# Kernel tuning notes

Measured on AMD Instinct MI355X. Metric: run time of the kernel, lower is better.

The kernel has to match this reference:

```python
import jax, jax.numpy as jnp
import numpy as np

N, E, F_IN, H, L = 1536, 49152, 27, 64, 32


def _ln(x, g, b, eps=1e-5):
    m = x.mean(-1, keepdims=True)
    v = ((x - m) ** 2).mean(-1, keepdims=True)
    return (x - m) * jax.lax.rsqrt(v + eps) * g + b


def _gatv2(x, src, dst, Wl, bl, Wr, br, att, bias, n):
    # PyG GATv2Conv, heads=1: alpha_ij = softmax_j( att . leaky_relu(Wl x_j + Wr x_i) )
    xl = x @ Wl + bl  # source transform [n,H]
    xr = x @ Wr + br  # target transform [n,H]
    e = jax.nn.leaky_relu(xl[src] + xr[dst], 0.2)  # [E',H]
    s = e @ att  # [E'] attention logits
    m = jax.ops.segment_max(s, dst, num_segments=n)
    w = jnp.exp(s - m[dst])
    denom = jax.ops.segment_sum(w, dst, num_segments=n)
    alpha = w / denom[dst]
    return jax.ops.segment_sum(alpha[:, None] * xl[src], dst, num_segments=n) + bias


def _model(x, eps_nodes, eps_graph, edge_index,
           Wl1, bl1, Wr1, br1, att1, bias1,
           Wl2, bl2, Wr2, br2, att2, bias2,
           Wnm, bnm, Wnv, bnv, Wgm, bgm, Wgv, bgv,
           Wd1, bd1, ln1_g, ln1_b, Wd2, bd2, ln2_g, ln2_b, Wd3, bd3,
           We1, be1, lne_g, lne_b, We2, be2,
           Wf1, bf1, lnf_g, lnf_b, Wf2, bf2):
    n = x.shape[0]
    loop = jnp.arange(n)
    src = jnp.concatenate([edge_index[0], loop])  # add self loops (PyG default)
    dst = jnp.concatenate([edge_index[1], loop])
    h = jax.nn.relu(_gatv2(x, src, dst, Wl1, bl1, Wr1, br1, att1, bias1, n))
    h = jax.nn.relu(_gatv2(h, src, dst, Wl2, bl2, Wr2, br2, att2, bias2, n))
    node_mu = h @ Wnm + bnm
    node_logvar = h @ Wnv + bnv
    gh = h.mean(0)
    graph_mu = gh @ Wgm + bgm
    graph_logvar = gh @ Wgv + bgv
    z = node_mu + eps_nodes * jnp.exp(0.5 * node_logvar)  # node reparam (training)
    _zg = graph_mu + eps_graph * jnp.exp(0.5 * graph_logvar)  # z_graph: computed, unused downstream as in source
    # dec_node_features MLP
    nf = _ln(jax.nn.relu(z @ Wd1 + bd1), ln1_g, ln1_b)
    nf = _ln(jax.nn.relu(nf @ Wd2 + bd2), ln2_g, ln2_b)
    nf = nf @ Wd3 + bd3  # [n, F_IN]
    # feature_refinement (node_embeddings = h is passed in forward)
    nf = _ln(jax.nn.relu(jnp.concatenate([nf, h], -1) @ Wf1 + bf1), lnf_g, lnf_b)
    node_features = nf @ Wf2 + bf2
    # edge_pred over all i<j pairs, vectorized (replaces the O(N^2) python loop)
    iu, ju = jnp.triu_indices(n, k=1)
    ei = jnp.concatenate([z[iu], z[ju]], -1)  # [P, 2L]
    eh = _ln(jax.nn.relu(ei @ We1 + be1), lne_g, lne_b)
    edge_logits = (eh @ We2 + be2)[:, 0]  # [P]
    return node_features, edge_logits, node_mu, node_logvar, graph_mu, graph_logvar


def setup_inputs() -> dict:
    key = jax.random.key(0)
    ki = iter(jax.random.split(key, 40))
    def W(fi, fo):
        return jax.random.normal(next(ki), (fi, fo), jnp.float32) / np.sqrt(fi)
    z64 = jnp.zeros((H,), jnp.float32)
    o64 = jnp.ones((H,), jnp.float32)
    zL = jnp.zeros((L,), jnp.float32)
    zF = jnp.zeros((F_IN,), jnp.float32)
    inp = {}
    inp["x"] = jax.random.normal(next(ki), (N, F_IN), jnp.float32)
    inp["edge_index"] = jax.random.randint(next(ki), (2, E), 0, N)
    inp["eps_nodes"] = jax.random.normal(next(ki), (N, L), jnp.float32)
    inp["eps_graph"] = jax.random.normal(next(ki), (L,), jnp.float32)
    inp.update(Wl1=W(F_IN, H), bl1=z64, Wr1=W(F_IN, H), br1=z64,
               att1=jax.random.normal(next(ki), (H,), jnp.float32) / np.sqrt(H), bias1=z64,
               Wl2=W(H, H), bl2=z64, Wr2=W(H, H), br2=z64,
               att2=jax.random.normal(next(ki), (H,), jnp.float32) / np.sqrt(H), bias2=z64)
    inp.update(Wnm=W(H, L), bnm=zL, Wnv=W(H, L), bnv=zL,
               Wgm=W(H, L), bgm=zL, Wgv=W(H, L), bgv=zL)
    inp.update(Wd1=W(L, H), bd1=z64, ln1_g=o64, ln1_b=z64,
               Wd2=W(H, H), bd2=z64, ln2_g=o64, ln2_b=z64,
               Wd3=W(H, F_IN), bd3=zF)
    inp.update(We1=W(2 * L, H), be1=z64, lne_g=o64, lne_b=z64,
               We2=W(H, 1), be2=jnp.zeros((1,), jnp.float32))
    inp.update(Wf1=W(F_IN + H, H), bf1=z64, lnf_g=o64, lnf_b=z64,
               Wf2=W(H, F_IN), bf2=zF)
    return inp


def reference(x, edge_index, eps_nodes, eps_graph,
              Wl1, bl1, Wr1, br1, att1, bias1,
              Wl2, bl2, Wr2, br2, att2, bias2,
              Wnm, bnm, Wnv, bnv, Wgm, bgm, Wgv, bgv,
              Wd1, bd1, ln1_g, ln1_b, Wd2, bd2, ln2_g, ln2_b, Wd3, bd3,
              We1, be1, lne_g, lne_b, We2, be2,
              Wf1, bf1, lnf_g, lnf_b, Wf2, bf2):
    return _model(x, eps_nodes, eps_graph, edge_index,
                  Wl1, bl1, Wr1, br1, att1, bias1,
                  Wl2, bl2, Wr2, br2, att2, bias2,
                  Wnm, bnm, Wnv, bnv, Wgm, bgm, Wgv, bgv,
                  Wd1, bd1, ln1_g, ln1_b, Wd2, bd2, ln2_g, ln2_b, Wd3, bd3,
                  We1, be1, lne_g, lne_b, We2, be2,
                  Wf1, bf1, lnf_g, lnf_b, Wf2, bf2)
```

## Files before the change

kernel.cpp:

```cpp
#include <hip/hip_runtime.h>

#define NN 1536
#define NE 49152
#define FIN 27
#define HD 64
#define LDIM 32
#define PP 1178880
#define CAP 128

#define EL_OFF  (NN*FIN)
#define MU_OFF  (EL_OFF + PP)
#define LV_OFF  (MU_OFF + NN*LDIM)
#define GMU_OFF (LV_OFF + NN*LDIM)
#define GLV_OFF (GMU_OFF + LDIM)

__device__ __forceinline__ float wsum(float v) {
#pragma unroll
  for (int m = 1; m < 64; m <<= 1) v += __shfl_xor(v, m, 64);
  return v;
}
__device__ __forceinline__ void wsum2(float& a, float& b) {
#pragma unroll
  for (int m = 1; m < 64; m <<= 1) {
    a += __shfl_xor(a, m, 64);
    b += __shfl_xor(b, m, 64);
  }
}
__device__ __forceinline__ void wsum4(float& a, float& b, float& c, float& d) {
#pragma unroll
  for (int m = 1; m < 64; m <<= 1) {
    a += __shfl_xor(a, m, 64);
    b += __shfl_xor(b, m, 64);
    c += __shfl_xor(c, m, 64);
    d += __shfl_xor(d, m, 64);
  }
}
__device__ __forceinline__ float lnorm64(float x, float g, float b) {
  float s1 = x, s2 = x * x;
  wsum2(s1, s2);
  float mu = s1 * (1.0f / 64.0f);
  float var = fmaf(-mu, mu, s2 * (1.0f / 64.0f));
  return (x - mu) * rsqrtf(var + 1e-5f) * g + b;
}
__device__ __forceinline__ void cp4(float* dst, const float* __restrict__ src,
                                    int n4, int t) {
  const float4* s4 = (const float4*)src;
  float4* d4 = (float4*)dst;
  for (int e = t; e < n4; e += 256) d4[e] = s4[e];
}

__device__ __forceinline__ float gat_gather(const int* __restrict__ cnt,
                                            const int* __restrict__ slot,
                                            const float* __restrict__ xl,
                                            float xri, float ak, int i, int k) {
  int n = min(cnt[i], CAP);
  const int* srow = slot + i * CAP;
  float acc = 0.f, den = 0.f;
  for (int e0 = 0; e0 < n; e0 += 64) {
    int sidx = (e0 + k < n) ? srow[e0 + k] : 0;
    int nn = min(64, n - e0);
    int j = 0;
    for (; j + 3 < nn; j += 4) {
      int s0 = __shfl(sidx, j, 64),     s1 = __shfl(sidx, j + 1, 64);
      int s2 = __shfl(sidx, j + 2, 64), s3 = __shfl(sidx, j + 3, 64);
      float x0 = xl[s0 * HD + k], x1 = xl[s1 * HD + k];
      float x2 = xl[s2 * HD + k], x3 = xl[s3 * HD + k];
      float e0v = x0 + xri, e1v = x1 + xri, e2v = x2 + xri, e3v = x3 + xri;
      e0v = fmaxf(e0v, 0.2f * e0v);
      e1v = fmaxf(e1v, 0.2f * e1v);
      e2v = fmaxf(e2v, 0.2f * e2v);
      e3v = fmaxf(e3v, 0.2f * e3v);
      float p0 = e0v * ak, p1 = e1v * ak, p2 = e2v * ak, p3 = e3v * ak;
      wsum4(p0, p1, p2, p3);
      float w0 = expf(p0), w1 = expf(p1), w2 = expf(p2), w3 = expf(p3);
      acc = fmaf(w0, x0, acc); den += w0;
      acc = fmaf(w1, x1, acc); den += w1;
      acc = fmaf(w2, x2, acc); den += w2;
      acc = fmaf(w3, x3, acc); den += w3;
    }
    for (; j < nn; ++j) {
      int s0 = __shfl(sidx, j, 64);
      float x0 = xl[s0 * HD + k];
      float e0v = x0 + xri;
      e0v = fmaxf(e0v, 0.2f * e0v);
      float w0 = expf(wsum(e0v * ak));
      acc = fmaf(w0, x0, acc); den += w0;
    }
  }
  float xs = xl[i * HD + k];
  float es = xs + xri;
  es = fmaxf(es, 0.2f * es);
  float ws = expf(wsum(es * ak));
  acc = fmaf(ws, xs, acc); den += ws;
  return acc / den;
}

__global__ __launch_bounds__(256) void gvae_xform1(
    const float* __restrict__ in,
    const float* __restrict__ Wl, const float* __restrict__ bl,
    const float* __restrict__ Wr, const float* __restrict__ br,
    float* __restrict__ xl, float* __restrict__ xr,
    const int* __restrict__ ei, int* __restrict__ cnt, int* __restrict__ slot) {
  __shared__ __align__(16) float sWl[FIN * HD];
  __shared__ __align__(16) float sWr[FIN * HD];
  int t = threadIdx.x;
  int gid = blockIdx.x * 256 + t;
  if (gid < NE) {
    int d = ei[NE + gid];
    int c = atomicAdd(&cnt[d], 1);
    if (c < CAP) slot[d * CAP + c] = ei[gid];
  }
  cp4(sWl, Wl, FIN * 16, t);
  cp4(sWr, Wr, FIN * 16, t);
  int i = blockIdx.x * 4 + (t >> 6);
  int k = t & 63;
  float xv = (k < FIN) ? in[i * FIN + k] : 0.f;
  float l0 = bl[k], l1 = 0.f, r0 = br[k], r1 = 0.f;
  __syncthreads();
#pragma unroll
  for (int a = 0; a < FIN; a += 2) {
    float xa = __shfl(xv, a, 64);
    l0 = fmaf(xa, sWl[a * HD + k], l0);
    r0 = fmaf(xa, sWr[a * HD + k], r0);
    if (a + 1 < FIN) {
      float xb = __shfl(xv, a + 1, 64);
      l1 = fmaf(xb, sWl[(a + 1) * HD + k], l1);
      r1 = fmaf(xb, sWr[(a + 1) * HD + k], r1);
    }
  }
  xl[i * HD + k] = l0 + l1;
  xr[i * HD + k] = r0 + r1;
}

__global__ __launch_bounds__(256) void gvae_gatherx(
    const int* __restrict__ cnt, const int* __restrict__ slot,
    const float* __restrict__ xl, const float* __restrict__ xr,
    const float* __restrict__ att, const float* __restrict__ hbias,
    const float* __restrict__ Wl, const float* __restrict__ bl,
    const float* __restrict__ Wr, const float* __restrict__ br,
    float* __restrict__ xlo, float* __restrict__ xro) {
  int t = threadIdx.x;
  int i = blockIdx.x * 4 + (t >> 6);
  int k = t & 63;
  float xri = xr[i * HD + k];
  float ak = att[k];
  float hv = fmaxf(gat_gather(cnt, slot, xl, xri, ak, i, k) + hbias[k], 0.f);
  float l0 = bl[k], l1 = 0.f, r0 = br[k], r1 = 0.f;
#pragma unroll
  for (int a = 0; a < HD; a += 2) {
    float xa = __shfl(hv, a, 64);
    float xb = __shfl(hv, a + 1, 64);
    l0 = fmaf(xa, Wl[a * HD + k], l0);
    r0 = fmaf(xa, Wr[a * HD + k], r0);
    l1 = fmaf(xb, Wl[(a + 1) * HD + k], l1);
    r1 = fmaf(xb, Wr[(a + 1) * HD + k], r1);
  }
  xlo[i * HD + k] = l0 + l1;
  xro[i * HD + k] = r0 + r1;
}

__global__ __launch_bounds__(256, 4) void gvae_node(
    const int* __restrict__ cnt, const int* __restrict__ slot,
    const float* __restrict__ xl, const float* __restrict__ xr,
    const float* __restrict__ att, const float* __restrict__ bias2,
    const float* __restrict__ eps,
    const float* __restrict__ Wnm, const float* __restrict__ bnm,
    const float* __restrict__ Wnv, const float* __restrict__ bnv,
    const float* __restrict__ We1, const float* __restrict__ be1,
    const float* __restrict__ Wd1, const float* __restrict__ bd1,
    const float* __restrict__ g1, const float* __restrict__ b1,
    const float* __restrict__ Wd2, const float* __restrict__ bd2,
    const float* __restrict__ g2, const float* __restrict__ b2,
    const float* __restrict__ Wd3, const float* __restrict__ bd3,
    const float* __restrict__ Wf1, const float* __restrict__ bf1,
    const float* __restrict__ gf, const float* __restrict__ bfv,
    const float* __restrict__ Wf2, const float* __restrict__ bf2,
    float* __restrict__ uo, float* __restrict__ vo,
    float* __restrict__ gh, float* __restrict__ out) {
  __shared__ float ghred[256];
  int t = threadIdx.x;
  int i = blockIdx.x * 4 + (t >> 6);
  int k = t & 63;
  int kk = k & 31;
  int kc = (k < FIN) ? k : (FIN - 1);

  float xri = xr[i * HD + k];
  float ak = att[k];
  float h2k = fmaxf(gat_gather(cnt, slot, xl, xri, ak, i, k) + bias2[k], 0.f);
  ghred[t] = h2k;
  __syncthreads();
  if (t < 64) {
    float s = (ghred[t] + ghred[t + 64]) + (ghred[t + 128] + ghred[t + 192]);
    atomicAdd(&gh[t], s * (1.0f / NN));
  }

  const float* W = (k < 32) ? Wnm : Wnv;
  float c0 = (k < 32) ? bnm[kk] : bnv[kk];
  float c1 = 0.f, c2 = 0.f, c3 = 0.f;
#pragma unroll
  for (int a = 0; a < HD; a += 4) {
    c0 = fmaf(__shfl(h2k, a, 64),     W[a * LDIM + kk],       c0);
    c1 = fmaf(__shfl(h2k, a + 1, 64), W[(a + 1) * LDIM + kk], c1);
    c2 = fmaf(__shfl(h2k, a + 2, 64), W[(a + 2) * LDIM + kk], c2);
    c3 = fmaf(__shfl(h2k, a + 3, 64), W[(a + 3) * LDIM + kk], c3);
  }
  float acc = (c0 + c1) + (c2 + c3);
  if (k < 32) out[MU_OFF + i * LDIM + kk] = acc;
  else        out[LV_OFF + i * LDIM + kk] = acc;

  float lv = __shfl(acc, k + 32, 64);
  float zk = acc + eps[i * LDIM + kk] * expf(0.5f * lv);

  float u0 = be1[k], u1 = 0.f, v0 = 0.f, v1 = 0.f;
#pragma unroll
  for (int a = 0; a < LDIM; a += 2) {
    float za = __shfl(zk, a, 64);
    float zb = __shfl(zk, a + 1, 64);
    u0 = fmaf(za, We1[a * HD + k], u0);
    u1 = fmaf(zb, We1[(a + 1) * HD + k], u1);
    v0 = fmaf(za, We1[(a + LDIM) * HD + k], v0);
    v1 = fmaf(zb, We1[(a + 1 + LDIM) * HD + k], v1);
  }
  uo[i * HD + k] = u0 + u1;
  vo[i * HD + k] = v0 + v1;

  c0 = bd1[k]; c1 = 0.f; c2 = 0.f; c3 = 0.f;
#pragma unroll
  for (int a = 0; a < LDIM; a += 4) {
    c0 = fmaf(__shfl(zk, a, 64),     Wd1[a * HD + k],       c0);
    c1 = fmaf(__shfl(zk, a + 1, 64), Wd1[(a + 1) * HD + k], c1);
    c2 = fmaf(__shfl(zk, a + 2, 64), Wd1[(a + 2) * HD + k], c2);
    c3 = fmaf(__shfl(zk, a + 3, 64), Wd1[(a + 3) * HD + k], c3);
  }
  float nf1 = lnorm64(fmaxf((c0 + c1) + (c2 + c3), 0.f), g1[k], b1[k]);

  c0 = bd2[k]; c1 = 0.f; c2 = 0.f; c3 = 0.f;
#pragma unroll
  for (int a = 0; a < HD; a += 4) {
    c0 = fmaf(__shfl(nf1, a, 64),     Wd2[a * HD + k],       c0);
    c1 = fmaf(__shfl(nf1, a + 1, 64), Wd2[(a + 1) * HD + k], c1);
    c2 = fmaf(__shfl(nf1, a + 2, 64), Wd2[(a + 2) * HD + k], c2);
    c3 = fmaf(__shfl(nf1, a + 3, 64), Wd2[(a + 3) * HD + k], c3);
  }
  float nf2 = lnorm64(fmaxf((c0 + c1) + (c2 + c3), 0.f), g2[k], b2[k]);

  c0 = 0.f; c1 = 0.f; c2 = 0.f; c3 = 0.f;
#pragma unroll
  for (int a = 0; a < HD; a += 4) {
    c0 = fmaf(__shfl(nf2, a, 64),     Wd3[a * FIN + kc],       c0);
    c1 = fmaf(__shfl(nf2, a + 1, 64), Wd3[(a + 1) * FIN + kc], c1);
    c2 = fmaf(__shfl(nf2, a + 2, 64), Wd3[(a + 2) * FIN + kc], c2);
    c3 = fmaf(__shfl(nf2, a + 3, 64), Wd3[(a + 3) * FIN + kc], c3);
  }
  float nf3 = (k < FIN) ? ((c0 + c1) + (c2 + c3) + bd3[kc]) : 0.f;

  c0 = bf1[k]; c1 = 0.f; c2 = 0.f; c3 = 0.f;
#pragma unroll
  for (int j = 0; j < FIN; j++) {
    float nj = __shfl(nf3, j, 64);
    c0 = fmaf(nj, Wf1[j * HD + k], c0);
  }
#pragma unroll
  for (int a = 0; a < HD; a += 4) {
    c0 = fmaf(__shfl(h2k, a, 64),     Wf1[(FIN + a) * HD + k],     c0);
    c1 = fmaf(__shfl(h2k, a + 1, 64), Wf1[(FIN + a + 1) * HD + k], c1);
    c2 = fmaf(__shfl(h2k, a + 2, 64), Wf1[(FIN + a + 2) * HD + k], c2);
    c3 = fmaf(__shfl(h2k, a + 3, 64), Wf1[(FIN + a + 3) * HD + k], c3);
  }
  float rr = lnorm64(fmaxf((c0 + c1) + (c2 + c3), 0.f), gf[k], bfv[k]);

  c0 = 0.f; c1 = 0.f; c2 = 0.f; c3 = 0.f;
#pragma unroll
  for (int a = 0; a < HD; a += 4) {
    c0 = fmaf(__shfl(rr, a, 64),     Wf2[a * FIN + kc],       c0);
    c1 = fmaf(__shfl(rr, a + 1, 64), Wf2[(a + 1) * FIN + kc], c1);
    c2 = fmaf(__shfl(rr, a + 2, 64), Wf2[(a + 2) * FIN + kc], c2);
    c3 = fmaf(__shfl(rr, a + 3, 64), Wf2[(a + 3) * FIN + kc], c3);
  }
  if (k < FIN) out[i * FIN + k] = (c0 + c1) + (c2 + c3) + bf2[kc];
}

__global__ __launch_bounds__(256) void gvae_edge(
    const float* __restrict__ u, const float* __restrict__ v,
    const float* __restrict__ lng, const float* __restrict__ lnb,
    const float* __restrict__ w2, const float* __restrict__ be2,
    const float* __restrict__ gh,
    const float* __restrict__ Wgm, const float* __restrict__ bgm,
    const float* __restrict__ Wgv, const float* __restrict__ bgv,
    float* __restrict__ out) {
  __shared__ float U[64 * 64];
  __shared__ float V[64 * 68];
  __shared__ float C[64];
  __shared__ float cc[2];
  int t = threadIdx.x;
  int wv = t >> 6, lane = t & 63;

  if (blockIdx.x == 0 && wv == 3) {
    int kk = lane & 31;
    float ghk = gh[lane];
    const float* W = (lane < 32) ? Wgm : Wgv;
    float c0 = (lane < 32) ? bgm[kk] : bgv[kk];
    float c1 = 0.f, c2 = 0.f, c3 = 0.f;
#pragma unroll
    for (int a = 0; a < HD; a += 4) {
      c0 = fmaf(__shfl(ghk, a, 64),     W[a * LDIM + kk],       c0);
      c1 = fmaf(__shfl(ghk, a + 1, 64), W[(a + 1) * LDIM + kk], c1);
      c2 = fmaf(__shfl(ghk, a + 2, 64), W[(a + 2) * LDIM + kk], c2);
      c3 = fmaf(__shfl(ghk, a + 3, 64), W[(a + 3) * LDIM + kk], c3);
    }
    float acc = (c0 + c1) + (c2 + c3);
    if (lane < 32) out[GMU_OFF + kk] = acc;
    else           out[GLV_OFF + kk] = acc;
  }

  int rem = blockIdx.x, bi = 0;
  while (rem >= 24 - bi) { rem -= 24 - bi; bi++; }
  int bj = bi + rem;

  const float4* u4p = (const float4*)(u + bi * 64 * HD);
  const float4* v4p = (const float4*)(v + bj * 64 * HD);
#pragma unroll
  for (int it = 0; it < 4; ++it) {
    int r = t + it * 256;
    int row = r >> 4, q = r & 15;
    float4 uu = u4p[r];
    *(float4*)&U[row * 64 + q * 4] = uu;
    float4 vv = v4p[r];
    *(float4*)&V[row * 68 + q * 4] = vv;
  }
  if (t < 64) {
    float ck = lng[t] * w2[t];
    C[t] = ck;
    float cb = lnb[t] * w2[t];
    float sC = wsum(ck);
    float sB = wsum(cb);
    if (t == 0) { cc[0] = sC; cc[1] = sB + be2[0]; }
  }
  __syncthreads();
  float C1 = cc[0], C0 = cc[1];

  float S1[16], S2[16], Sc[16];
#pragma unroll
  for (int ii = 0; ii < 16; ii++) { S1[ii] = 0.f; S2[ii] = 0.f; Sc[ii] = 0.f; }
  const float* Ub = &U[(wv * 16) * 64];
  for (int k4 = 0; k4 < 16; k4++) {
    float4 v4 = *(const float4*)&V[lane * 68 + k4 * 4];
    float4 c4 = *(const float4*)&C[k4 * 4];
#pragma unroll
    for (int ii = 0; ii < 16; ii++) {
      float4 u4 = *(const float4*)&Ub[ii * 64 + k4 * 4];
      float t0 = fmaxf(u4.x + v4.x, 0.f);
      float t1 = fmaxf(u4.y + v4.y, 0.f);
      float t2 = fmaxf(u4.z + v4.z, 0.f);
      float t3 = fmaxf(u4.w + v4.w, 0.f);
      S1[ii] += (t0 + t1) + (t2 + t3);
      S2[ii] = fmaf(t0, t0, fmaf(t1, t1, fmaf(t2, t2, fmaf(t3, t3, S2[ii]))));
      Sc[ii] = fmaf(t0, c4.x, fmaf(t1, c4.y, fmaf(t2, c4.z, fmaf(t3, c4.w, Sc[ii]))));
    }
  }
  int j = bj * 64 + lane;
  const float inv64 = 1.0f / 64.0f;
#pragma unroll
  for (int ii = 0; ii < 16; ii++) {
    int i = bi * 64 + wv * 16 + ii;
    if (j > i) {
      int pbase = i * (2 * NN - i - 1) / 2 - i - 1;
      float mu = S1[ii] * inv64;
      float var = fmaf(-mu, mu, S2[ii] * inv64);
      float logit = (Sc[ii] - mu * C1) * rsqrtf(var + 1e-5f) + C0;
      out[EL_OFF + pbase + j] = logit;
    }
  }
}

extern "C" void kernel_launch(void* const* d_in, const int* in_sizes, int n_in,
                              void* d_out, int out_size, void* d_ws, size_t ws_size,
                              hipStream_t stream) {
  const float* x    = (const float*)d_in[0];
  const int*   ei   = (const int*)d_in[1];
  const float* eps  = (const float*)d_in[2];
  const float* Wl1  = (const float*)d_in[4];
  const float* bl1  = (const float*)d_in[5];
  const float* Wr1  = (const float*)d_in[6];
  const float* br1  = (const float*)d_in[7];
  const float* att1 = (const float*)d_in[8];
  const float* bias1= (const float*)d_in[9];
  const float* Wl2  = (const float*)d_in[10];
  const float* bl2  = (const float*)d_in[11];
  const float* Wr2  = (const float*)d_in[12];
  const float* br2  = (const float*)d_in[13];
  const float* att2 = (const float*)d_in[14];
  const float* bias2= (const float*)d_in[15];
  const float* Wnm  = (const float*)d_in[16];
  const float* bnm  = (const float*)d_in[17];
  const float* Wnv  = (const float*)d_in[18];
  const float* bnv  = (const float*)d_in[19];
  const float* Wgm  = (const float*)d_in[20];
  const float* bgm  = (const float*)d_in[21];
  const float* Wgv  = (const float*)d_in[22];
  const float* bgv  = (const float*)d_in[23];
  const float* Wd1  = (const float*)d_in[24];
  const float* bd1  = (const float*)d_in[25];
  const float* ln1g = (const float*)d_in[26];
  const float* ln1b = (const float*)d_in[27];
  const float* Wd2  = (const float*)d_in[28];
  const float* bd2  = (const float*)d_in[29];
  const float* ln2g = (const float*)d_in[30];
  const float* ln2b = (const float*)d_in[31];
  const float* Wd3  = (const float*)d_in[32];
  const float* bd3  = (const float*)d_in[33];
  const float* We1  = (const float*)d_in[34];
  const float* be1  = (const float*)d_in[35];
  const float* lneg = (const float*)d_in[36];
  const float* lneb = (const float*)d_in[37];
  const float* We2  = (const float*)d_in[38];
  const float* be2  = (const float*)d_in[39];
  const float* Wf1  = (const float*)d_in[40];
  const float* bf1  = (const float*)d_in[41];
  const float* lnfg = (const float*)d_in[42];
  const float* lnfb = (const float*)d_in[43];
  const float* Wf2  = (const float*)d_in[44];
  const float* bf2  = (const float*)d_in[45];
  float* out = (float*)d_out;

  float* fb  = (float*)d_ws;
  float* xl1 = fb;
  float* xr1 = xl1 + NN * HD;
  float* xl2 = xr1 + NN * HD;
  float* xr2 = xl2 + NN * HD;
  float* uu  = xr2 + NN * HD;
  float* vv  = uu  + NN * HD;
  float* gh  = vv  + NN * HD;
  int* cnt    = (int*)(gh + HD);
  int* slot   = cnt + NN;

  hipMemsetAsync(gh, 0, (HD + NN) * sizeof(float), stream);

  gvae_xform1<<<NN / 4, 256, 0, stream>>>(x, Wl1, bl1, Wr1, br1, xl1, xr1,
                                          ei, cnt, slot);
  gvae_gatherx<<<NN / 4, 256, 0, stream>>>(cnt, slot, xl1, xr1, att1, bias1,
                                           Wl2, bl2, Wr2, br2, xl2, xr2);
  gvae_node<<<NN / 4, 256, 0, stream>>>(cnt, slot, xl2, xr2, att2, bias2, eps,
      Wnm, bnm, Wnv, bnv, We1, be1,
      Wd1, bd1, ln1g, ln1b, Wd2, bd2, ln2g, ln2b, Wd3, bd3,
      Wf1, bf1, lnfg, lnfb, Wf2, bf2,
      uu, vv, gh, out);
  gvae_edge<<<300, 256, 0, stream>>>(uu, vv, lneg, lneb, We2, be2,
                                     gh, Wgm, bgm, Wgv, bgv, out);
}
```

Baseline: 222.1 us.

## Move decoder MLP into edge kernel and shrink edge tiles to 16x64

The decoder and refinement MLP chain moves out of the node kernel into extra blocks of the edge kernel. The node kernel now writes h2 and z to workspace, so it gets shorter and the MLP work can run alongside the edge tiles. The edge kernel is retiled from 300 blocks of 64x64 to 1200 blocks of 16x64. U rows are held in registers and broadcast with shuffles instead of being staged in LDS, which gives more blocks and less register pressure per block. The cost is extra global traffic for h2 and z, more V reloads across the smaller tiles, and shuffle overhead in the inner loop.

```diff
diff --git a/kernel.cpp b/kernel.cpp
--- a/kernel.cpp
+++ b/kernel.cpp
@@ -7,6 +7,7 @@
 #define LDIM 32
 #define PP 1178880
 #define CAP 128
+#define NTILE 1200
 
 #define EL_OFF  (NN*FIN)
 #define MU_OFF  (EL_OFF + PP)
@@ -167,6 +168,66 @@
     const float* __restrict__ Wnm, const float* __restrict__ bnm,
     const float* __restrict__ Wnv, const float* __restrict__ bnv,
     const float* __restrict__ We1, const float* __restrict__ be1,
+    float* __restrict__ uo, float* __restrict__ vo,
+    float* __restrict__ h2o, float* __restrict__ zzo,
+    float* __restrict__ gh, float* __restrict__ out) {
+  __shared__ float ghred[256];
+  int t = threadIdx.x;
+  int i = blockIdx.x * 4 + (t >> 6);
+  int k = t & 63;
+  int kk = k & 31;
+
+  float xri = xr[i * HD + k];
+  float ak = att[k];
+  float h2k = fmaxf(gat_gather(cnt, slot, xl, xri, ak, i, k) + bias2[k], 0.f);
+  h2o[i * HD + k] = h2k;
+  ghred[t] = h2k;
+  __syncthreads();
+  if (t < 64) {
+    float s = (ghred[t] + ghred[t + 64]) + (ghred[t + 128] + ghred[t + 192]);
+    atomicAdd(&gh[t], s * (1.0f / NN));
+  }
+
+  const float* W = (k < 32) ? Wnm : Wnv;
+  float c0 = (k < 32) ? bnm[kk] : bnv[kk];
+  float c1 = 0.f, c2 = 0.f, c3 = 0.f;
+#pragma unroll
+  for (int a = 0; a < HD; a += 4) {
+    c0 = fmaf(__shfl(h2k, a, 64),     W[a * LDIM + kk],       c0);
+    c1 = fmaf(__shfl(h2k, a + 1, 64), W[(a + 1) * LDIM + kk], c1);
+    c2 = fmaf(__shfl(h2k, a + 2, 64), W[(a + 2) * LDIM + kk], c2);
+    c3 = fmaf(__shfl(h2k, a + 3, 64), W[(a + 3) * LDIM + kk], c3);
+  }
+  float acc = (c0 + c1) + (c2 + c3);
+  if (k < 32) out[MU_OFF + i * LDIM + kk] = acc;
+  else        out[LV_OFF + i * LDIM + kk] = acc;
+
+  float lv = __shfl(acc, k + 32, 64);
+  float zk = acc + eps[i * LDIM + kk] * expf(0.5f * lv);
+  if (k < 32) zzo[i * LDIM + kk] = zk;
+
+  float u0 = be1[k], u1 = 0.f, v0 = 0.f, v1 = 0.f;
+#pragma unroll
+  for (int a = 0; a < LDIM; a += 2) {
+    float za = __shfl(zk, a, 64);
+    float zb = __shfl(zk, a + 1, 64);
+    u0 = fmaf(za, We1[a * HD + k], u0);
+    u1 = fmaf(zb, We1[(a + 1) * HD + k], u1);
+    v0 = fmaf(za, We1[(a + LDIM) * HD + k], v0);
+    v1 = fmaf(zb, We1[(a + 1 + LDIM) * HD + k], v1);
+  }
+  uo[i * HD + k] = u0 + u1;
+  vo[i * HD + k] = v0 + v1;
+}
+
+__global__ __launch_bounds__(256) void gvae_edge(
+    const float* __restrict__ u, const float* __restrict__ v,
+    const float* __restrict__ lng, const float* __restrict__ lnb,
+    const float* __restrict__ w2, const float* __restrict__ be2,
+    const float* __restrict__ gh,
+    const float* __restrict__ Wgm, const float* __restrict__ bgm,
+    const float* __restrict__ Wgv, const float* __restrict__ bgv,
+    const float* __restrict__ h2, const float* __restrict__ zz,
     const float* __restrict__ Wd1, const float* __restrict__ bd1,
     const float* __restrict__ g1, const float* __restrict__ b1,
     const float* __restrict__ Wd2, const float* __restrict__ bd2,
@@ -175,127 +236,79 @@
     const float* __restrict__ Wf1, const float* __restrict__ bf1,
     const float* __restrict__ gf, const float* __restrict__ bfv,
     const float* __restrict__ Wf2, const float* __restrict__ bf2,
-    float* __restrict__ uo, float* __restrict__ vo,
-    float* __restrict__ gh, float* __restrict__ out) {
-  __shared__ float ghred[256];
-  int t = threadIdx.x;
-  int i = blockIdx.x * 4 + (t >> 6);
-  int k = t & 63;
-  int kk = k & 31;
-  int kc = (k < FIN) ? k : (FIN - 1);
-
-  float xri = xr[i * HD + k];
-  float ak = att[k];
-  float h2k = fmaxf(gat_gather(cnt, slot, xl, xri, ak, i, k) + bias2[k], 0.f);
-  ghred[t] = h2k;
-  __syncthreads();
-  if (t < 64) {
-    float s = (ghred[t] + ghred[t + 64]) + (ghred[t + 128] + ghred[t + 192]);
-    atomicAdd(&gh[t], s * (1.0f / NN));
-  }
-
-  const float* W = (k < 32) ? Wnm : Wnv;
-  float c0 = (k < 32) ? bnm[kk] : bnv[kk];
-  float c1 = 0.f, c2 = 0.f, c3 = 0.f;
-#pragma unroll
-  for (int a = 0; a < HD; a += 4) {
-    c0 = fmaf(__shfl(h2k, a, 64),     W[a * LDIM + kk],       c0);
-    c1 = fmaf(__shfl(h2k, a + 1, 64), W[(a + 1) * LDIM + kk], c1);
-    c2 = fmaf(__shfl(h2k, a + 2, 64), W[(a + 2) * LDIM + kk], c2);
-    c3 = fmaf(__shfl(h2k, a + 3, 64), W[(a + 3) * LDIM + kk], c3);
-  }
-  float acc = (c0 + c1) + (c2 + c3);
-  if (k < 32) out[MU_OFF + i * LDIM + kk] = acc;
-  else        out[LV_OFF + i * LDIM + kk] = acc;
-
-  float lv = __shfl(acc, k + 32, 64);
-  float zk = acc + eps[i * LDIM + kk] * expf(0.5f * lv);
-
-  float u0 = be1[k], u1 = 0.f, v0 = 0.f, v1 = 0.f;
-#pragma unroll
-  for (int a = 0; a < LDIM; a += 2) {
-    float za = __shfl(zk, a, 64);
-    float zb = __shfl(zk, a + 1, 64);
-    u0 = fmaf(za, We1[a * HD + k], u0);
-    u1 = fmaf(zb, We1[(a + 1) * HD + k], u1);
-    v0 = fmaf(za, We1[(a + LDIM) * HD + k], v0);
-    v1 = fmaf(zb, We1[(a + 1 + LDIM) * HD + k], v1);
-  }
-  uo[i * HD + k] = u0 + u1;
-  vo[i * HD + k] = v0 + v1;
-
-  c0 = bd1[k]; c1 = 0.f; c2 = 0.f; c3 = 0.f;
-#pragma unroll
-  for (int a = 0; a < LDIM; a += 4) {
-    c0 = fmaf(__shfl(zk, a, 64),     Wd1[a * HD + k],       c0);
-    c1 = fmaf(__shfl(zk, a + 1, 64), Wd1[(a + 1) * HD + k], c1);
-    c2 = fmaf(__shfl(zk, a + 2, 64), Wd1[(a + 2) * HD + k], c2);
-    c3 = fmaf(__shfl(zk, a + 3, 64), Wd1[(a + 3) * HD + k], c3);
-  }
-  float nf1 = lnorm64(fmaxf((c0 + c1) + (c2 + c3), 0.f), g1[k], b1[k]);
-
-  c0 = bd2[k]; c1 = 0.f; c2 = 0.f; c3 = 0.f;
-#pragma unroll
-  for (int a = 0; a < HD; a += 4) {
-    c0 = fmaf(__shfl(nf1, a, 64),     Wd2[a * HD + k],       c0);
-    c1 = fmaf(__shfl(nf1, a + 1, 64), Wd2[(a + 1) * HD + k], c1);
-    c2 = fmaf(__shfl(nf1, a + 2, 64), Wd2[(a + 2) * HD + k], c2);
-    c3 = fmaf(__shfl(nf1, a + 3, 64), Wd2[(a + 3) * HD + k], c3);
-  }
-  float nf2 = lnorm64(fmaxf((c0 + c1) + (c2 + c3), 0.f), g2[k], b2[k]);
-
-  c0 = 0.f; c1 = 0.f; c2 = 0.f; c3 = 0.f;
-#pragma unroll
-  for (int a = 0; a < HD; a += 4) {
-    c0 = fmaf(__shfl(nf2, a, 64),     Wd3[a * FIN + kc],       c0);
-    c1 = fmaf(__shfl(nf2, a + 1, 64), Wd3[(a + 1) * FIN + kc], c1);
-    c2 = fmaf(__shfl(nf2, a + 2, 64), Wd3[(a + 2) * FIN + kc], c2);
-    c3 = fmaf(__shfl(nf2, a + 3, 64), Wd3[(a + 3) * FIN + kc], c3);
-  }
-  float nf3 = (k < FIN) ? ((c0 + c1) + (c2 + c3) + bd3[kc]) : 0.f;
-
-  c0 = bf1[k]; c1 = 0.f; c2 = 0.f; c3 = 0.f;
-#pragma unroll
-  for (int j = 0; j < FIN; j++) {
-    float nj = __shfl(nf3, j, 64);
-    c0 = fmaf(nj, Wf1[j * HD + k], c0);
-  }
-#pragma unroll
-  for (int a = 0; a < HD; a += 4) {
-    c0 = fmaf(__shfl(h2k, a, 64),     Wf1[(FIN + a) * HD + k],     c0);
-    c1 = fmaf(__shfl(h2k, a + 1, 64), Wf1[(FIN + a + 1) * HD + k], c1);
-    c2 = fmaf(__shfl(h2k, a + 2, 64), Wf1[(FIN + a + 2) * HD + k], c2);
-    c3 = fmaf(__shfl(h2k, a + 3, 64), Wf1[(FIN + a + 3) * HD + k], c3);
-  }
-  float rr = lnorm64(fmaxf((c0 + c1) + (c2 + c3), 0.f), gf[k], bfv[k]);
-
-  c0 = 0.f; c1 = 0.f; c2 = 0.f; c3 = 0.f;
-#pragma unroll
-  for (int a = 0; a < HD; a += 4) {
-    c0 = fmaf(__shfl(rr, a, 64),     Wf2[a * FIN + kc],       c0);
-    c1 = fmaf(__shfl(rr, a + 1, 64), Wf2[(a + 1) * FIN + kc], c1);
-    c2 = fmaf(__shfl(rr, a + 2, 64), Wf2[(a + 2) * FIN + kc], c2);
-    c3 = fmaf(__shfl(rr, a + 3, 64), Wf2[(a + 3) * FIN + kc], c3);
-  }
-  if (k < FIN) out[i * FIN + k] = (c0 + c1) + (c2 + c3) + bf2[kc];
-}
-
-__global__ __launch_bounds__(256) void gvae_edge(
-    const float* __restrict__ u, const float* __restrict__ v,
-    const float* __restrict__ lng, const float* __restrict__ lnb,
-    const float* __restrict__ w2, const float* __restrict__ be2,
-    const float* __restrict__ gh,
-    const float* __restrict__ Wgm, const float* __restrict__ bgm,
-    const float* __restrict__ Wgv, const float* __restrict__ bgv,
     float* __restrict__ out) {
-  __shared__ float U[64 * 64];
   __shared__ float V[64 * 68];
   __shared__ float C[64];
   __shared__ float cc[2];
   int t = threadIdx.x;
+  int b = blockIdx.x;
   int wv = t >> 6, lane = t & 63;
 
-  if (blockIdx.x == 0 && wv == 3) {
+  if (b >= NTILE) {
+    int i = (b - NTILE) * 4 + wv;
+    int k = lane;
+    int kc = (k < FIN) ? k : (FIN - 1);
+    float h2k = h2[i * HD + k];
+    float zk = zz[i * LDIM + (k & 31)];
+
+    float c0 = bd1[k], c1 = 0.f, c2 = 0.f, c3 = 0.f;
+#pragma unroll
+    for (int a = 0; a < LDIM; a += 4) {
+      c0 = fmaf(__shfl(zk, a, 64),     Wd1[a * HD + k],       c0);
+      c1 = fmaf(__shfl(zk, a + 1, 64), Wd1[(a + 1) * HD + k], c1);
+      c2 = fmaf(__shfl(zk, a + 2, 64), Wd1[(a + 2) * HD + k], c2);
+      c3 = fmaf(__shfl(zk, a + 3, 64), Wd1[(a + 3) * HD + k], c3);
+    }
+    float nf1 = lnorm64(fmaxf((c0 + c1) + (c2 + c3), 0.f), g1[k], b1[k]);
+
+    c0 = bd2[k]; c1 = 0.f; c2 = 0.f; c3 = 0.f;
+#pragma unroll
+    for (int a = 0; a < HD; a += 4) {
+      c0 = fmaf(__shfl(nf1, a, 64),     Wd2[a * HD + k],       c0);
+      c1 = fmaf(__shfl(nf1, a + 1, 64), Wd2[(a + 1) * HD + k], c1);
+      c2 = fmaf(__shfl(nf1, a + 2, 64), Wd2[(a + 2) * HD + k], c2);
+      c3 = fmaf(__shfl(nf1, a + 3, 64), Wd2[(a + 3) * HD + k], c3);
+    }
+    float nf2 = lnorm64(fmaxf((c0 + c1) + (c2 + c3), 0.f), g2[k], b2[k]);
+
+    c0 = 0.f; c1 = 0.f; c2 = 0.f; c3 = 0.f;
+#pragma unroll
+    for (int a = 0; a < HD; a += 4) {
+      c0 = fmaf(__shfl(nf2, a, 64),     Wd3[a * FIN + kc],       c0);
+      c1 = fmaf(__shfl(nf2, a + 1, 64), Wd3[(a + 1) * FIN + kc], c1);
+      c2 = fmaf(__shfl(nf2, a + 2, 64), Wd3[(a + 2) * FIN + kc], c2);
+      c3 = fmaf(__shfl(nf2, a + 3, 64), Wd3[(a + 3) * FIN + kc], c3);
+    }
+    float nf3 = (k < FIN) ? ((c0 + c1) + (c2 + c3) + bd3[kc]) : 0.f;
+
+    c0 = bf1[k]; c1 = 0.f; c2 = 0.f; c3 = 0.f;
+#pragma unroll
+    for (int j = 0; j < FIN; j++) {
+      float nj = __shfl(nf3, j, 64);
+      c0 = fmaf(nj, Wf1[j * HD + k], c0);
+    }
+#pragma unroll
+    for (int a = 0; a < HD; a += 4) {
+      c0 = fmaf(__shfl(h2k, a, 64),     Wf1[(FIN + a) * HD + k],     c0);
+      c1 = fmaf(__shfl(h2k, a + 1, 64), Wf1[(FIN + a + 1) * HD + k], c1);
+      c2 = fmaf(__shfl(h2k, a + 2, 64), Wf1[(FIN + a + 2) * HD + k], c2);
+      c3 = fmaf(__shfl(h2k, a + 3, 64), Wf1[(FIN + a + 3) * HD + k], c3);
+    }
+    float rr = lnorm64(fmaxf((c0 + c1) + (c2 + c3), 0.f), gf[k], bfv[k]);
+
+    c0 = 0.f; c1 = 0.f; c2 = 0.f; c3 = 0.f;
+#pragma unroll
+    for (int a = 0; a < HD; a += 4) {
+      c0 = fmaf(__shfl(rr, a, 64),     Wf2[a * FIN + kc],       c0);
+      c1 = fmaf(__shfl(rr, a + 1, 64), Wf2[(a + 1) * FIN + kc], c1);
+      c2 = fmaf(__shfl(rr, a + 2, 64), Wf2[(a + 2) * FIN + kc], c2);
+      c3 = fmaf(__shfl(rr, a + 3, 64), Wf2[(a + 3) * FIN + kc], c3);
+    }
+    if (k < FIN) out[i * FIN + k] = (c0 + c1) + (c2 + c3) + bf2[kc];
+    return;
+  }
+
+  if (b == 0 && wv == 3) {
     int kk = lane & 31;
     float ghk = gh[lane];
     const float* W = (lane < 32) ? Wgm : Wgv;
@@ -313,18 +326,20 @@
     else           out[GLV_OFF + kk] = acc;
   }
 
-  int rem = blockIdx.x, bi = 0;
-  while (rem >= 24 - bi) { rem -= 24 - bi; bi++; }
-  int bj = bi + rem;
-
-  const float4* u4p = (const float4*)(u + bi * 64 * HD);
-  const float4* v4p = (const float4*)(v + bj * 64 * HD);
+  int rem = b, cg = 0;
+  while (rem >= 4 * (cg + 1)) { rem -= 4 * (cg + 1); cg++; }
+  int rg = rem;
+
+  float Ureg[4];
+#pragma unroll
+  for (int q = 0; q < 4; ++q)
+    Ureg[q] = u[(rg * 16 + wv * 4 + q) * HD + lane];
+
+  const float4* v4p = (const float4*)(v + cg * 64 * HD);
 #pragma unroll
   for (int it = 0; it < 4; ++it) {
     int r = t + it * 256;
     int row = r >> 4, q = r & 15;
-    float4 uu = u4p[r];
-    *(float4*)&U[row * 64 + q * 4] = uu;
     float4 vv = v4p[r];
     *(float4*)&V[row * 68 + q * 4] = vv;
   }
@@ -339,35 +354,37 @@
   __syncthreads();
   float C1 = cc[0], C0 = cc[1];
 
-  float S1[16], S2[16], Sc[16];
-#pragma unroll
-  for (int ii = 0; ii < 16; ii++) { S1[ii] = 0.f; S2[ii] = 0.f; Sc[ii] = 0.f; }
-  const float* Ub = &U[(wv * 16) * 64];
+  float S1[4], S2[4], Sc[4];
+#pragma unroll
+  for (int q = 0; q < 4; q++) { S1[q] = 0.f; S2[q] = 0.f; Sc[q] = 0.f; }
   for (int k4 = 0; k4 < 16; k4++) {
     float4 v4 = *(const float4*)&V[lane * 68 + k4 * 4];
     float4 c4 = *(const float4*)&C[k4 * 4];
 #pragma unroll
-    for (int ii = 0; ii < 16; ii++) {
-      float4 u4 = *(const float4*)&Ub[ii * 64 + k4 * 4];
-      float t0 = fmaxf(u4.x + v4.x, 0.f);
-      float t1 = fmaxf(u4.y + v4.y, 0.f);
-      float t2 = fmaxf(u4.z + v4.z, 0.f);
-      float t3 = fmaxf(u4.w + v4.w, 0.f);
-      S1[ii] += (t0 + t1) + (t2 + t3);
-      S2[ii] = fmaf(t0, t0, fmaf(t1, t1, fmaf(t2, t2, fmaf(t3, t3, S2[ii]))));
-      Sc[ii] = fmaf(t0, c4.x, fmaf(t1, c4.y, fmaf(t2, c4.z, fmaf(t3, c4.w, Sc[ii]))));
-    }
-  }
-  int j = bj * 64 + lane;
+    for (int q = 0; q < 4; q++) {
+      float u0 = __shfl(Ureg[q], k4 * 4, 64);
+      float u1 = __shfl(Ureg[q], k4 * 4 + 1, 64);
+      float u2 = __shfl(Ureg[q], k4 * 4 + 2, 64);
+      float u3 = __shfl(Ureg[q], k4 * 4 + 3, 64);
+      float t0 = fmaxf(u0 + v4.x, 0.f);
+      float t1 = fmaxf(u1 + v4.y, 0.f);
+      float t2 = fmaxf(u2 + v4.z, 0.f);
+      float t3 = fmaxf(u3 + v4.w, 0.f);
+      S1[q] += (t0 + t1) + (t2 + t3);
+      S2[q] = fmaf(t0, t0, fmaf(t1, t1, fmaf(t2, t2, fmaf(t3, t3, S2[q]))));
+      Sc[q] = fmaf(t0, c4.x, fmaf(t1, c4.y, fmaf(t2, c4.z, fmaf(t3, c4.w, Sc[q]))));
+    }
+  }
+  int j = cg * 64 + lane;
   const float inv64 = 1.0f / 64.0f;
 #pragma unroll
-  for (int ii = 0; ii < 16; ii++) {
-    int i = bi * 64 + wv * 16 + ii;
+  for (int q = 0; q < 4; q++) {
+    int i = rg * 16 + wv * 4 + q;
     if (j > i) {
       int pbase = i * (2 * NN - i - 1) / 2 - i - 1;
-      float mu = S1[ii] * inv64;
-      float var = fmaf(-mu, mu, S2[ii] * inv64);
-      float logit = (Sc[ii] - mu * C1) * rsqrtf(var + 1e-5f) + C0;
+      float mu = S1[q] * inv64;
+      float var = fmaf(-mu, mu, S2[q] * inv64);
+      float logit = (Sc[q] - mu * C1) * rsqrtf(var + 1e-5f) + C0;
       out[EL_OFF + pbase + j] = logit;
     }
   }
@@ -430,7 +447,9 @@
   float* xr2 = xl2 + NN * HD;
   float* uu  = xr2 + NN * HD;
   float* vv  = uu  + NN * HD;
-  float* gh  = vv  + NN * HD;
+  float* h2  = vv  + NN * HD;
+  float* zz  = h2  + NN * HD;
+  float* gh  = zz  + NN * LDIM;
   int* cnt    = (int*)(gh + HD);
   int* slot   = cnt + NN;
 
@@ -442,9 +461,11 @@
                                            Wl2, bl2, Wr2, br2, xl2, xr2);
   gvae_node<<<NN / 4, 256, 0, stream>>>(cnt, slot, xl2, xr2, att2, bias2, eps,
       Wnm, bnm, Wnv, bnv, We1, be1,
+      uu, vv, h2, zz, gh, out);
+  gvae_edge<<<NTILE + NN / 4, 256, 0, stream>>>(uu, vv, lneg, lneb, We2, be2,
+      gh, Wgm, bgm, Wgv, bgv,
+      h2, zz,
       Wd1, bd1, ln1g, ln1b, Wd2, bd2, ln2g, ln2b, Wd3, bd3,
       Wf1, bf1, lnfg, lnfb, Wf2, bf2,
-      uu, vv, gh, out);
-  gvae_edge<<<300, 256, 0, stream>>>(uu, vv, lneg, lneb, We2, be2,
-                                     gh, Wgm, bgm, Wgv, bgv, out);
-}
+      out);
+}
```

Result: no change. 225.2 us (+1.4%).
